# Kernel tuning notes

Hardware: AMD Instinct MI355X
Metric: run time of the kernel (lower is better)

Reference implementation:

```python
import jax, jax.numpy as jnp
import numpy as np

S, B, C, H = 8192, 4, 512, 8
D = C // H
EPS = 1e-6


def setup_inputs() -> dict:
    key = jax.random.key(0)
    ks = jax.random.split(key, 11)
    scale = 1.0 / np.sqrt(C)
    return {
        "query": jax.random.normal(ks[0], (S, B, C), jnp.float32),
        "key": jax.random.normal(ks[1], (S, B, C), jnp.float32),
        "value": jax.random.normal(ks[2], (S, B, C), jnp.float32),
        "Wq": jax.random.normal(ks[3], (C, C), jnp.float32) * scale,
        "bq": jnp.zeros((C,), jnp.float32),
        "Wk": jax.random.normal(ks[4], (C, C), jnp.float32) * scale,
        "bk": jnp.zeros((C,), jnp.float32),
        "Wv": jax.random.normal(ks[5], (C, C), jnp.float32) * scale,
        "bv": jnp.zeros((C,), jnp.float32),
        "Wp": jax.random.normal(ks[6], (C, C), jnp.float32) * scale,
        "bp": jnp.zeros((C,), jnp.float32),
    }


def _elu_fm(x):
    # ELU(x) + 1 feature map
    return jax.nn.elu(x) + 1.0


def _heads(x, W, b):
    # x: [B, N, C] -> [B, H, N, D]
    y = x @ W.T + b
    Bb, N, _ = y.shape
    return y.reshape(Bb, N, H, D).transpose(0, 2, 1, 3)


def reference(query, key, value, Wq, bq, Wk, bk, Wv, bv, Wp, bp):
    # inputs [S, B, C] -> batch-first [B, S, C]
    q_in = query.transpose(1, 0, 2)
    k_in = key.transpose(1, 0, 2)
    v_in = value.transpose(1, 0, 2)

    q = _elu_fm(_heads(q_in, Wq, bq))   # [B,H,N,D]
    k = _elu_fm(_heads(k_in, Wk, bk))   # [B,H,N,D]
    v = _heads(v_in, Wv, bv)            # [B,H,N,D]

    # linear attention: O(N) kv-sum formulation
    kv = jnp.einsum('bhnd,bhnf->bhdf', k, v)       # [B,H,D,D]
    k_sum = k.sum(axis=2)                          # [B,H,D]
    qkv = jnp.einsum('bhnd,bhdf->bhnf', q, kv)     # [B,H,N,D]
    denom = jnp.einsum('bhnd,bhd->bhn', q, k_sum)  # [B,H,N]
    y = qkv / (denom[..., None] + EPS)

    # merge heads, output projection, back to [S, B, C]
    y = y.transpose(0, 2, 1, 3).reshape(q_in.shape[0], q_in.shape[1], C)
    out = y @ Wp.T + bp
    return out.transpose(1, 0, 2)
```

## Files before the change

kernel.cpp:

```cpp
#include <hip/hip_runtime.h>
#include <hip/hip_bf16.h>
#include <math.h>

#define S_LEN 8192
#define BATCH 4
#define CDIM  512
#define HEADS 8
#define DDIM  64
#define MROWS (S_LEN * BATCH)
#define EPS_F 1e-6f

typedef __attribute__((ext_vector_type(8))) short     short8_t;
typedef __attribute__((ext_vector_type(4))) float     f32x4;
typedef unsigned short ushort_t;
typedef __attribute__((ext_vector_type(4))) unsigned short ushort4_t;
typedef __attribute__((ext_vector_type(8))) unsigned short ushort8_t;

static __device__ __forceinline__ ushort_t f2bf(float f) {
  __hip_bfloat16 h = __float2bfloat16(f);
  return *(ushort_t*)&h;
}

static __device__ __forceinline__ void gl2lds16(const ushort_t* g, ushort_t* l) {
  __builtin_amdgcn_global_load_lds((const __attribute__((address_space(1))) void*)g,
                                   (__attribute__((address_space(3))) void*)l,
                                   16, 0, 0);
}

__global__ __launch_bounds__(256)
void cvtW_kernel(const float* __restrict__ a, const float* __restrict__ b,
                 const float* __restrict__ c, const float* __restrict__ d,
                 ushort_t* __restrict__ oa, ushort_t* __restrict__ ob,
                 ushort_t* __restrict__ oc, ushort_t* __restrict__ od) {
  const float* src = (blockIdx.y == 0) ? a : (blockIdx.y == 1) ? b :
                     (blockIdx.y == 2) ? c : d;
  ushort_t* dst    = (blockIdx.y == 0) ? oa : (blockIdx.y == 1) ? ob :
                     (blockIdx.y == 2) ? oc : od;
  const size_t i = ((size_t)blockIdx.x * 256 + threadIdx.x) * 8;
  const float4 x = *(const float4*)&src[i];
  const float4 y = *(const float4*)&src[i + 4];
  ushort8_t p;
  p[0] = f2bf(x.x); p[1] = f2bf(x.y); p[2] = f2bf(x.z); p[3] = f2bf(x.w);
  p[4] = f2bf(y.x); p[5] = f2bf(y.y); p[6] = f2bf(y.z); p[7] = f2bf(y.w);
  *(ushort8_t*)&dst[i] = p;
}

template<int AF32, int OUTF32>
static __device__ __forceinline__
void rowpanel_body(const void* __restrict__ Av, const ushort_t* __restrict__ BT,
                   const float* __restrict__ bias, void* __restrict__ Yv,
                   const bool act, const int m0, ushort_t (*blds)[8192]) {
  const int t    = threadIdx.x;
  const int w    = t >> 6;
  const int lane = t & 63;
  const int lr   = lane & 15;
  const int lk   = (lane >> 4) * 8;
  const int arow = m0 + w * 16 + lr;

  const float*    Af = (const float*)Av;
  const ushort_t* Ah = (const ushort_t*)Av;

  short8_t afr[16];
  #pragma unroll
  for (int kf = 0; kf < 16; ++kf) {
    if (AF32) {
      const float4 x0 = *(const float4*)&Af[(size_t)arow * CDIM + kf * 32 + lk];
      const float4 x1 = *(const float4*)&Af[(size_t)arow * CDIM + kf * 32 + lk + 4];
      short8_t v;
      v[0] = (short)f2bf(x0.x); v[1] = (short)f2bf(x0.y);
      v[2] = (short)f2bf(x0.z); v[3] = (short)f2bf(x0.w);
      v[4] = (short)f2bf(x1.x); v[5] = (short)f2bf(x1.y);
      v[6] = (short)f2bf(x1.z); v[7] = (short)f2bf(x1.w);
      afr[kf] = v;
    } else {
      afr[kf] = *(const short8_t*)&Ah[(size_t)arow * CDIM + kf * 32 + lk];
    }
  }

  for (int nt = 0; nt < 4; ++nt) {
    const int n0 = nt * 128;
    f32x4 acc[8];
    #pragma unroll
    for (int nf = 0; nf < 8; ++nf) acc[nf] = (f32x4){0.f, 0.f, 0.f, 0.f};

    auto stageB = [&](int buf, int ks) {
      #pragma unroll
      for (int i = 0; i < 4; ++i) {
        const int fid = w * 4 + i;
        const int k2 = fid >> 3, nf = fid & 7;
        gl2lds16(BT + (size_t)(n0 + nf * 16 + lr) * CDIM + ks * 64 + k2 * 32 + lk,
                 &blds[buf][fid * 512]);
      }
    };

    stageB(0, 0);
    int cur = 0;
    #pragma unroll
    for (int ks = 0; ks < 8; ++ks) {
      __syncthreads();
      if (ks < 7) stageB(cur ^ 1, ks + 1);
      #pragma unroll
      for (int k2 = 0; k2 < 2; ++k2) {
        short8_t bfr[8];
        #pragma unroll
        for (int nf = 0; nf < 8; ++nf)
          bfr[nf] = *(const short8_t*)&blds[cur][(k2 * 8 + nf) * 512 + lane * 8];
        #pragma unroll
        for (int nf = 0; nf < 8; ++nf)
          acc[nf] = __builtin_amdgcn_mfma_f32_16x16x32_bf16(
              afr[ks * 2 + k2], bfr[nf], acc[nf], 0, 0, 0);
      }
      cur ^= 1;
    }

    float* Yf = (float*)Yv;
    ushort_t* Yh = (ushort_t*)Yv;
    #pragma unroll
    for (int nf = 0; nf < 8; ++nf) {
      const int col = n0 + nf * 16 + lr;
      const float bi = bias[col];
      #pragma unroll
      for (int r = 0; r < 4; ++r) {
        const int m = m0 + w * 16 + (lane >> 4) * 4 + r;
        float vv = acc[nf][r] + bi;
        if (act) vv = (vv > 0.f) ? (vv + 1.f) : expf(vv);
        if (OUTF32) Yf[(size_t)m * CDIM + col] = vv;
        else        Yh[(size_t)m * CDIM + col] = f2bf(vv);
      }
    }
  }
}

__global__ __launch_bounds__(256)
void proj3_rowpanel(const float* __restrict__ Xq, const float* __restrict__ Xk,
                    const float* __restrict__ Xv,
                    const ushort_t* __restrict__ Wq, const ushort_t* __restrict__ Wk,
                    const ushort_t* __restrict__ Wv,
                    const float* __restrict__ bq, const float* __restrict__ bk,
                    const float* __restrict__ bv,
                    ushort_t* __restrict__ Yq, ushort_t* __restrict__ Yk,
                    ushort_t* __restrict__ Yv) {
  __shared__ __align__(16) ushort_t blds[2][8192];
  const int z = blockIdx.y;
  const float*    X    = (z == 0) ? Xq : (z == 1) ? Xk : Xv;
  const ushort_t* BT   = (z == 0) ? Wq : (z == 1) ? Wk : Wv;
  const float*    bias = (z == 0) ? bq : (z == 1) ? bk : bv;
  ushort_t*       Y    = (z == 0) ? Yq : (z == 1) ? Yk : Yv;
  rowpanel_body<1, 0>(X, BT, bias, Y, z < 2, blockIdx.x * 64, blds);
}

__global__ __launch_bounds__(256)
void outp_rowpanel(const ushort_t* __restrict__ A, const ushort_t* __restrict__ BT,
                   const float* __restrict__ bias, float* __restrict__ Y) {
  __shared__ __align__(16) ushort_t blds[2][8192];
  rowpanel_body<0, 1>(A, BT, bias, Y, false, blockIdx.x * 64, blds);
}

__global__ __launch_bounds__(256)
void gemm_kv(const ushort_t* __restrict__ Kb, const ushort_t* __restrict__ Vb,
             float* __restrict__ kvpart, float* __restrict__ ksumpart) {
  __shared__ __align__(16) ushort_t klds[8192];
  __shared__ __align__(16) ushort_t vlds[8192];
  const int bh    = blockIdx.x;
  const int chunk = blockIdx.y;
  const int b = bh >> 3, h = bh & 7;
  const int t = threadIdx.x;
  const int w = t >> 6;
  const int lane = t & 63;

  f32x4 acc[4];
  #pragma unroll
  for (int fg = 0; fg < 4; ++fg) acc[fg] = (f32x4){0.f, 0.f, 0.f, 0.f};
  f32x4 accs = (f32x4){0.f, 0.f, 0.f, 0.f};

  short8_t ones;
  #pragma unroll
  for (int i = 0; i < 8; ++i) ones[i] = (short)0x3F80;

  for (int round = 0; round < 4; ++round) {
    const int sbase = chunk * 512 + round * 128;
    __syncthreads();
    #pragma unroll
    for (int i = 0; i < 4; ++i) {
      const int idx  = i * 256 + t;
      const int sl   = idx >> 3;
      const int d8   = idx & 7;
      const size_t src = (size_t)((sbase + sl) * BATCH + b) * CDIM + h * DDIM + d8 * 8;
      const ushort8_t kp = *(const ushort8_t*)&Kb[src];
      const ushort8_t vp = *(const ushort8_t*)&Vb[src];
      const int sb  = sl >> 5;
      const int j   = sl & 7;
      const int lp0 = (d8 & 1) * 8 + ((sl >> 3) & 3) * 16;
      const int dg  = d8 >> 1;
      const int kbase = ((sb * 4 + dg) * 64 + lp0) * 8 + j;
      #pragma unroll
      for (int e = 0; e < 8; ++e) {
        klds[kbase + e * 8] = kp[e];
        vlds[kbase + e * 8] = vp[e];
      }
    }
    __syncthreads();
    #pragma unroll
    for (int sb = 0; sb < 4; ++sb) {
      const short8_t af = *(const short8_t*)&klds[((sb * 4 + w) * 64 + lane) * 8];
      accs = __builtin_amdgcn_mfma_f32_16x16x32_bf16(af, ones, accs, 0, 0, 0);
      #pragma unroll
      for (int fg = 0; fg < 4; ++fg) {
        const short8_t bf = *(const short8_t*)&vlds[((sb * 4 + fg) * 64 + lane) * 8];
        acc[fg] = __builtin_amdgcn_mfma_f32_16x16x32_bf16(af, bf, acc[fg], 0, 0, 0);
      }
    }
  }

  const size_t obase = ((size_t)bh * 16 + chunk) * 64;
  #pragma unroll
  for (int fg = 0; fg < 4; ++fg)
    #pragma unroll
    for (int r = 0; r < 4; ++r) {
      const int d = w * 16 + (lane >> 4) * 4 + r;
      kvpart[(obase + d) * 64 + fg * 16 + (lane & 15)] = acc[fg][r];
    }
  if ((lane & 15) == 0) {
    #pragma unroll
    for (int r = 0; r < 4; ++r)
      ksumpart[obase + w * 16 + (lane >> 4) * 4 + r] = accs[r];
  }
}

__global__ __launch_bounds__(256)
void kv_finish(const float* __restrict__ kvpart, const float* __restrict__ ksumpart,
               ushort_t* __restrict__ kvT) {
  const int bh = blockIdx.x;
  const int t  = threadIdx.x;
  for (int idx = t; idx < 4096; idx += 256) {
    const int d = idx >> 6, f = idx & 63;
    float s = 0.f;
    for (int c = 0; c < 16; ++c)
      s += kvpart[(((size_t)bh * 16 + c) * 64 + d) * 64 + f];
    kvT[((size_t)bh * 80 + f) * 64 + d] = f2bf(s);
  }
  if (t < 64) {
    float s = 0.f;
    for (int c = 0; c < 16; ++c)
      s += ksumpart[((size_t)bh * 16 + c) * 64 + t];
    kvT[((size_t)bh * 80 + 64) * 64 + t] = f2bf(s);
  }
  for (int i = t; i < 15 * 64; i += 256)
    kvT[((size_t)bh * 80 + 65) * 64 + i] = 0;
}

__global__ __launch_bounds__(256)
void gemm_qkv(ushort_t* __restrict__ Qb, const ushort_t* __restrict__ kvT) {
  __shared__ __align__(16) ushort_t alds[8192];
  __shared__ __align__(16) ushort_t blds[5120];
  const int bh    = blockIdx.x;
  const int chunk = blockIdx.y;
  const int b = bh >> 3, h = bh & 7;
  const int t = threadIdx.x;
  const int w = t >> 6;
  const int lane = t & 63;
  const int lr = lane & 15;
  const int lk = (lane >> 4) * 8;

  #pragma unroll
  for (int i = 0; i < 4; ++i) {
    const int fidx = w * 4 + i;
    const int ks = fidx >> 3, fm = fidx & 7;
    const ushort_t* src = Qb +
        (size_t)((chunk * 128 + fm * 16 + lr) * BATCH + b) * CDIM +
        h * DDIM + ks * 32 + lk;
    gl2lds16(src, &alds[fidx * 512]);
  }
  for (int idx = w; idx < 10; idx += 4) {
    const int ks = idx / 5, fg = idx % 5;
    const ushort_t* src = kvT + (size_t)(bh * 80 + fg * 16 + lr) * 64 + ks * 32 + lk;
    gl2lds16(src, &blds[idx * 512]);
  }
  __syncthreads();

  f32x4 acc[2][5];
  #pragma unroll
  for (int mi = 0; mi < 2; ++mi)
    #pragma unroll
    for (int fg = 0; fg < 5; ++fg)
      acc[mi][fg] = (f32x4){0.f, 0.f, 0.f, 0.f};

  #pragma unroll
  for (int ks = 0; ks < 2; ++ks) {
    short8_t af[2], bf[5];
    #pragma unroll
    for (int mi = 0; mi < 2; ++mi)
      af[mi] = *(const short8_t*)&alds[(ks * 8 + w * 2 + mi) * 512 + lane * 8];
    #pragma unroll
    for (int fg = 0; fg < 5; ++fg)
      bf[fg] = *(const short8_t*)&blds[(ks * 5 + fg) * 512 + lane * 8];
    #pragma unroll
    for (int mi = 0; mi < 2; ++mi)
      #pragma unroll
      for (int fg = 0; fg < 5; ++fg)
        acc[mi][fg] = __builtin_amdgcn_mfma_f32_16x16x32_bf16(
            af[mi], bf[fg], acc[mi][fg], 0, 0, 0);
  }

  #pragma unroll
  for (int mi = 0; mi < 2; ++mi) {
    #pragma unroll
    for (int r = 0; r < 4; ++r) {
      const float dv  = __shfl(acc[mi][4][r], lane & 48);
      const float inv = 1.f / (dv + EPS_F);
      const int s = chunk * 128 + w * 32 + mi * 16 + (lane >> 4) * 4 + r;
      const size_t rowb = (size_t)(s * BATCH + b) * CDIM + h * DDIM;
      #pragma unroll
      for (int fg = 0; fg < 4; ++fg)
        Qb[rowb + fg * 16 + lr] = f2bf(acc[mi][fg][r] * inv);
    }
  }
}

extern "C" void kernel_launch(void* const* d_in, const int* in_sizes, int n_in,
                              void* d_out, int out_size, void* d_ws, size_t ws_size,
                              hipStream_t stream) {
  const float* q_in = (const float*)d_in[0];
  const float* k_in = (const float*)d_in[1];
  const float* v_in = (const float*)d_in[2];
  const float* Wq   = (const float*)d_in[3];
  const float* bq   = (const float*)d_in[4];
  const float* Wk   = (const float*)d_in[5];
  const float* bk   = (const float*)d_in[6];
  const float* Wv   = (const float*)d_in[7];
  const float* bv   = (const float*)d_in[8];
  const float* Wp   = (const float*)d_in[9];
  const float* bp   = (const float*)d_in[10];
  float* out = (float*)d_out;

  const size_t NTOK = (size_t)MROWS * CDIM;
  const size_t NW   = (size_t)CDIM * CDIM;
  ushort_t* Wq_bf  = (ushort_t*)d_ws;
  ushort_t* Wk_bf  = Wq_bf + NW;
  ushort_t* Wv_bf  = Wk_bf + NW;
  ushort_t* Wp_bf  = Wv_bf + NW;
  ushort_t* qbuf   = Wp_bf + NW;
  ushort_t* kbuf   = qbuf + NTOK;
  ushort_t* vbuf   = kbuf + NTOK;
  ushort_t* kvT    = vbuf + NTOK;
  float* kvpart    = (float*)(kvT + (size_t)32 * 80 * 64);
  float* ksumpart  = kvpart + (size_t)512 * 64 * 64;

  const dim3 blk(256);

  cvtW_kernel<<<dim3(128, 4), blk, 0, stream>>>(Wq, Wk, Wv, Wp,
                                                Wq_bf, Wk_bf, Wv_bf, Wp_bf);

  proj3_rowpanel<<<dim3(MROWS / 64, 3), blk, 0, stream>>>(
      q_in, k_in, v_in, Wq_bf, Wk_bf, Wv_bf, bq, bk, bv, qbuf, kbuf, vbuf);

  gemm_kv<<<dim3(32, 16), blk, 0, stream>>>(kbuf, vbuf, kvpart, ksumpart);
  kv_finish<<<dim3(32), blk, 0, stream>>>(kvpart, ksumpart, kvT);

  gemm_qkv<<<dim3(32, 64), blk, 0, stream>>>(qbuf, kvT);

  outp_rowpanel<<<dim3(MROWS / 64), blk, 0, stream>>>(qbuf, Wp_bf, bp, out);
}
```

Before: 239.5 us.

## Pre-pack weights into MFMA fragment layout and drop per-step barriers in projections

```diff
diff --git a/kernel.cpp b/kernel.cpp
--- a/kernel.cpp
+++ b/kernel.cpp
@@ -28,101 +28,89 @@
 }
 
 __global__ __launch_bounds__(256)
-void cvtW_kernel(const float* __restrict__ a, const float* __restrict__ b,
-                 const float* __restrict__ c, const float* __restrict__ d,
-                 ushort_t* __restrict__ oa, ushort_t* __restrict__ ob,
-                 ushort_t* __restrict__ oc, ushort_t* __restrict__ od) {
+void cvtW_pack(const float* __restrict__ a, const float* __restrict__ b,
+               const float* __restrict__ c, const float* __restrict__ d,
+               ushort_t* __restrict__ oa, ushort_t* __restrict__ ob,
+               ushort_t* __restrict__ oc, ushort_t* __restrict__ od) {
   const float* src = (blockIdx.y == 0) ? a : (blockIdx.y == 1) ? b :
                      (blockIdx.y == 2) ? c : d;
   ushort_t* dst    = (blockIdx.y == 0) ? oa : (blockIdx.y == 1) ? ob :
                      (blockIdx.y == 2) ? oc : od;
   const size_t i = ((size_t)blockIdx.x * 256 + threadIdx.x) * 8;
+  const int n  = (int)(i >> 9);
+  const int k0 = (int)(i & 511);
   const float4 x = *(const float4*)&src[i];
   const float4 y = *(const float4*)&src[i + 4];
   ushort8_t p;
   p[0] = f2bf(x.x); p[1] = f2bf(x.y); p[2] = f2bf(x.z); p[3] = f2bf(x.w);
   p[4] = f2bf(y.x); p[5] = f2bf(y.y); p[6] = f2bf(y.z); p[7] = f2bf(y.w);
-  *(ushort8_t*)&dst[i] = p;
-}
-
-template<int AF32, int OUTF32>
+  const int kf   = k0 >> 5;
+  const int lane = ((k0 >> 3) & 3) * 16 + (n & 15);
+  const int nfg  = n >> 4;
+  *(ushort8_t*)&dst[(((size_t)nfg * 16 + kf) * 64 + lane) * 8] = p;
+}
+
+template<int OUTF32>
 static __device__ __forceinline__
-void rowpanel_body(const void* __restrict__ Av, const ushort_t* __restrict__ BT,
+void nobar_compute(const ushort_t* __restrict__ alds,
+                   const ushort_t* __restrict__ Wpk,
                    const float* __restrict__ bias, void* __restrict__ Yv,
-                   const bool act, const int m0, ushort_t (*blds)[8192]) {
+                   const bool act, const int m0) {
   const int t    = threadIdx.x;
   const int w    = t >> 6;
   const int lane = t & 63;
-  const int lr   = lane & 15;
-  const int lk   = (lane >> 4) * 8;
-  const int arow = m0 + w * 16 + lr;
-
-  const float*    Af = (const float*)Av;
-  const ushort_t* Ah = (const ushort_t*)Av;
-
-  short8_t afr[16];
-  #pragma unroll
-  for (int kf = 0; kf < 16; ++kf) {
-    if (AF32) {
-      const float4 x0 = *(const float4*)&Af[(size_t)arow * CDIM + kf * 32 + lk];
-      const float4 x1 = *(const float4*)&Af[(size_t)arow * CDIM + kf * 32 + lk + 4];
-      short8_t v;
-      v[0] = (short)f2bf(x0.x); v[1] = (short)f2bf(x0.y);
-      v[2] = (short)f2bf(x0.z); v[3] = (short)f2bf(x0.w);
-      v[4] = (short)f2bf(x1.x); v[5] = (short)f2bf(x1.y);
-      v[6] = (short)f2bf(x1.z); v[7] = (short)f2bf(x1.w);
-      afr[kf] = v;
-    } else {
-      afr[kf] = *(const short8_t*)&Ah[(size_t)arow * CDIM + kf * 32 + lk];
-    }
-  }
-
-  for (int nt = 0; nt < 4; ++nt) {
-    const int n0 = nt * 128;
-    f32x4 acc[8];
-    #pragma unroll
-    for (int nf = 0; nf < 8; ++nf) acc[nf] = (f32x4){0.f, 0.f, 0.f, 0.f};
-
-    auto stageB = [&](int buf, int ks) {
-      #pragma unroll
-      for (int i = 0; i < 4; ++i) {
-        const int fid = w * 4 + i;
-        const int k2 = fid >> 3, nf = fid & 7;
-        gl2lds16(BT + (size_t)(n0 + nf * 16 + lr) * CDIM + ks * 64 + k2 * 32 + lk,
-                 &blds[buf][fid * 512]);
-      }
-    };
-
-    stageB(0, 0);
-    int cur = 0;
-    #pragma unroll
-    for (int ks = 0; ks < 8; ++ks) {
-      __syncthreads();
-      if (ks < 7) stageB(cur ^ 1, ks + 1);
-      #pragma unroll
-      for (int k2 = 0; k2 < 2; ++k2) {
-        short8_t bfr[8];
-        #pragma unroll
-        for (int nf = 0; nf < 8; ++nf)
-          bfr[nf] = *(const short8_t*)&blds[cur][(k2 * 8 + nf) * 512 + lane * 8];
-        #pragma unroll
-        for (int nf = 0; nf < 8; ++nf)
-          acc[nf] = __builtin_amdgcn_mfma_f32_16x16x32_bf16(
-              afr[ks * 2 + k2], bfr[nf], acc[nf], 0, 0, 0);
-      }
-      cur ^= 1;
-    }
-
-    float* Yf = (float*)Yv;
-    ushort_t* Yh = (ushort_t*)Yv;
-    #pragma unroll
-    for (int nf = 0; nf < 8; ++nf) {
-      const int col = n0 + nf * 16 + lr;
-      const float bi = bias[col];
+
+  f32x4 acc[4][8];
+  #pragma unroll
+  for (int mi = 0; mi < 4; ++mi)
+    #pragma unroll
+    for (int nf = 0; nf < 8; ++nf)
+      acc[mi][nf] = (f32x4){0.f, 0.f, 0.f, 0.f};
+
+  short8_t a_[4], b0[8], b1[8];
+
+  auto LB = [&](int kf, short8_t (&bb)[8]) {
+    #pragma unroll
+    for (int nf = 0; nf < 8; ++nf)
+      bb[nf] = *(const short8_t*)&Wpk[(((size_t)(w * 8 + nf) * 16 + kf) * 64 + lane) * 8];
+  };
+  auto LA = [&](int kf) {
+    #pragma unroll
+    for (int mi = 0; mi < 4; ++mi)
+      a_[mi] = *(const short8_t*)&alds[((kf * 4 + mi) * 64 + lane) * 8];
+  };
+  auto MF = [&](short8_t (&bb)[8]) {
+    #pragma unroll
+    for (int mi = 0; mi < 4; ++mi)
+      #pragma unroll
+      for (int nf = 0; nf < 8; ++nf)
+        acc[mi][nf] = __builtin_amdgcn_mfma_f32_16x16x32_bf16(
+            a_[mi], bb[nf], acc[mi][nf], 0, 0, 0);
+  };
+
+  LB(0, b0);
+  #pragma unroll
+  for (int kk = 0; kk < 8; ++kk) {
+    LB(kk * 2 + 1, b1);
+    LA(kk * 2);
+    MF(b0);
+    if (kk < 7) LB(kk * 2 + 2, b0);
+    LA(kk * 2 + 1);
+    MF(b1);
+  }
+
+  float* Yf = (float*)Yv;
+  ushort_t* Yh = (ushort_t*)Yv;
+  #pragma unroll
+  for (int nf = 0; nf < 8; ++nf) {
+    const int col = w * 128 + nf * 16 + (lane & 15);
+    const float bi = bias[col];
+    #pragma unroll
+    for (int mi = 0; mi < 4; ++mi) {
       #pragma unroll
       for (int r = 0; r < 4; ++r) {
-        const int m = m0 + w * 16 + (lane >> 4) * 4 + r;
-        float vv = acc[nf][r] + bi;
+        const int m = m0 + mi * 16 + (lane >> 4) * 4 + r;
+        float vv = acc[mi][nf][r] + bi;
         if (act) vv = (vv > 0.f) ? (vv + 1.f) : expf(vv);
         if (OUTF32) Yf[(size_t)m * CDIM + col] = vv;
         else        Yh[(size_t)m * CDIM + col] = f2bf(vv);
@@ -132,28 +120,64 @@
 }
 
 __global__ __launch_bounds__(256)
-void proj3_rowpanel(const float* __restrict__ Xq, const float* __restrict__ Xk,
-                    const float* __restrict__ Xv,
-                    const ushort_t* __restrict__ Wq, const ushort_t* __restrict__ Wk,
-                    const ushort_t* __restrict__ Wv,
-                    const float* __restrict__ bq, const float* __restrict__ bk,
-                    const float* __restrict__ bv,
-                    ushort_t* __restrict__ Yq, ushort_t* __restrict__ Yk,
-                    ushort_t* __restrict__ Yv) {
-  __shared__ __align__(16) ushort_t blds[2][8192];
+void proj3_nobar(const float* __restrict__ Xq, const float* __restrict__ Xk,
+                 const float* __restrict__ Xv,
+                 const ushort_t* __restrict__ Wqp, const ushort_t* __restrict__ Wkp,
+                 const ushort_t* __restrict__ Wvp,
+                 const float* __restrict__ bq, const float* __restrict__ bk,
+                 const float* __restrict__ bv,
+                 ushort_t* __restrict__ Yq, ushort_t* __restrict__ Yk,
+                 ushort_t* __restrict__ Yv) {
+  __shared__ __align__(16) ushort_t alds[32768];
   const int z = blockIdx.y;
   const float*    X    = (z == 0) ? Xq : (z == 1) ? Xk : Xv;
-  const ushort_t* BT   = (z == 0) ? Wq : (z == 1) ? Wk : Wv;
+  const ushort_t* Wpk  = (z == 0) ? Wqp : (z == 1) ? Wkp : Wvp;
   const float*    bias = (z == 0) ? bq : (z == 1) ? bk : bv;
   ushort_t*       Y    = (z == 0) ? Yq : (z == 1) ? Yk : Yv;
-  rowpanel_body<1, 0>(X, BT, bias, Y, z < 2, blockIdx.x * 64, blds);
-}
-
-__global__ __launch_bounds__(256)
-void outp_rowpanel(const ushort_t* __restrict__ A, const ushort_t* __restrict__ BT,
-                   const float* __restrict__ bias, float* __restrict__ Y) {
-  __shared__ __align__(16) ushort_t blds[2][8192];
-  rowpanel_body<0, 1>(A, BT, bias, Y, false, blockIdx.x * 64, blds);
+  const int t  = threadIdx.x;
+  const int m0 = blockIdx.x * 64;
+
+  #pragma unroll
+  for (int it = 0; it < 16; ++it) {
+    const int u   = it * 256 + t;
+    const int row = u >> 6;
+    const int k8  = u & 63;
+    const float4 x0 = *(const float4*)&X[(size_t)(m0 + row) * CDIM + k8 * 8];
+    const float4 x1 = *(const float4*)&X[(size_t)(m0 + row) * CDIM + k8 * 8 + 4];
+    short8_t v;
+    v[0] = (short)f2bf(x0.x); v[1] = (short)f2bf(x0.y);
+    v[2] = (short)f2bf(x0.z); v[3] = (short)f2bf(x0.w);
+    v[4] = (short)f2bf(x1.x); v[5] = (short)f2bf(x1.y);
+    v[6] = (short)f2bf(x1.z); v[7] = (short)f2bf(x1.w);
+    const int kf = k8 >> 2, mf = row >> 4;
+    const int ln = (k8 & 3) * 16 + (row & 15);
+    *(short8_t*)&alds[((kf * 4 + mf) * 64 + ln) * 8] = v;
+  }
+  __syncthreads();
+
+  nobar_compute<0>(alds, Wpk, bias, Y, z < 2, m0);
+}
+
+__global__ __launch_bounds__(256)
+void outp_nobar(const ushort_t* __restrict__ A, const ushort_t* __restrict__ Wpk,
+                const float* __restrict__ bias, float* __restrict__ Y) {
+  __shared__ __align__(16) ushort_t alds[32768];
+  const int t    = threadIdx.x;
+  const int w    = t >> 6;
+  const int lane = t & 63;
+  const int m0   = blockIdx.x * 64;
+
+  #pragma unroll
+  for (int j = 0; j < 16; ++j) {
+    const int fid = w * 16 + j;
+    const int kf = fid >> 2, mf = fid & 3;
+    const ushort_t* ga = A +
+        (size_t)(m0 + mf * 16 + (lane & 15)) * CDIM + kf * 32 + (lane >> 4) * 8;
+    gl2lds16(ga, (ushort_t*)&alds[fid * 512]);
+  }
+  __syncthreads();
+
+  nobar_compute<1>(alds, Wpk, bias, Y, false, m0);
 }
 
 __global__ __launch_bounds__(256)
@@ -335,11 +359,11 @@
 
   const size_t NTOK = (size_t)MROWS * CDIM;
   const size_t NW   = (size_t)CDIM * CDIM;
-  ushort_t* Wq_bf  = (ushort_t*)d_ws;
-  ushort_t* Wk_bf  = Wq_bf + NW;
-  ushort_t* Wv_bf  = Wk_bf + NW;
-  ushort_t* Wp_bf  = Wv_bf + NW;
-  ushort_t* qbuf   = Wp_bf + NW;
+  ushort_t* Wqp    = (ushort_t*)d_ws;
+  ushort_t* Wkp    = Wqp + NW;
+  ushort_t* Wvp    = Wkp + NW;
+  ushort_t* Wpp    = Wvp + NW;
+  ushort_t* qbuf   = Wpp + NW;
   ushort_t* kbuf   = qbuf + NTOK;
   ushort_t* vbuf   = kbuf + NTOK;
   ushort_t* kvT    = vbuf + NTOK;
@@ -348,16 +372,16 @@
 
   const dim3 blk(256);
 
-  cvtW_kernel<<<dim3(128, 4), blk, 0, stream>>>(Wq, Wk, Wv, Wp,
-                                                Wq_bf, Wk_bf, Wv_bf, Wp_bf);
-
-  proj3_rowpanel<<<dim3(MROWS / 64, 3), blk, 0, stream>>>(
-      q_in, k_in, v_in, Wq_bf, Wk_bf, Wv_bf, bq, bk, bv, qbuf, kbuf, vbuf);
+  cvtW_pack<<<dim3(128, 4), blk, 0, stream>>>(Wq, Wk, Wv, Wp,
+                                              Wqp, Wkp, Wvp, Wpp);
+
+  proj3_nobar<<<dim3(MROWS / 64, 3), blk, 0, stream>>>(
+      q_in, k_in, v_in, Wqp, Wkp, Wvp, bq, bk, bv, qbuf, kbuf, vbuf);
 
   gemm_kv<<<dim3(32, 16), blk, 0, stream>>>(kbuf, vbuf, kvpart, ksumpart);
   kv_finish<<<dim3(32), blk, 0, stream>>>(kvpart, ksumpart, kvT);
 
   gemm_qkv<<<dim3(32, 64), blk, 0, stream>>>(qbuf, kvT);
 
-  outp_rowpanel<<<dim3(MROWS / 64), blk, 0, stream>>>(qbuf, Wp_bf, bp, out);
-}
+  outp_nobar<<<dim3(MROWS / 64), blk, 0, stream>>>(qbuf, Wpp, bp, out);
+}
```

Result: faster. 234.4 us (-2.1%).
